# Kernel tuning notes

Hardware: AMD Instinct MI355X
Metric: run time of the kernel (lower is better)

## Reference

```python
import jax, jax.numpy as jnp
import numpy as np

B, N, DIM, HEADS, NBS = 64, 197, 768, 12, 10
WIN = (14, 14)
HEAD_DIM = DIM // HEADS
SCALE = HEAD_DIM ** -0.5


def _gen_relative_position_index():
    Wh, Ww = WIN
    num_rel = (2 * Wh - 1) * (2 * Ww - 1) + 3
    coords = np.stack(np.meshgrid(np.arange(Wh), np.arange(Ww), indexing='ij')).reshape(2, -1)
    rel = (coords[:, :, None] - coords[:, None, :]).transpose(1, 2, 0).astype(np.int32)
    rel[:, :, 0] += Wh - 1
    rel[:, :, 1] += Ww - 1
    rel[:, :, 0] *= 2 * Ww - 1
    idx = np.zeros((Wh * Ww + 1, Wh * Ww + 1), dtype=np.int32)
    idx[1:, 1:] = rel.sum(-1)
    idx[0, :] = num_rel - 3
    idx[:, 0] = num_rel - 2
    idx[0, 0] = num_rel - 1
    return jnp.asarray(idx)


def setup_inputs() -> dict:
    key = jax.random.key(0)
    ks = jax.random.split(key, 8)
    s = 0.02  # init scale for learned params
    return {
        'x': jax.random.normal(ks[0], (B, N, DIM), jnp.float32),
        'qkv_weight': jax.random.normal(ks[1], (3 * DIM, DIM), jnp.float32) * s,
        'q_bias': jax.random.normal(ks[2], (NBS, DIM), jnp.float32) * s,
        'v_bias': jax.random.normal(ks[3], (NBS, DIM), jnp.float32) * s,
        'rel_table': jax.random.normal(ks[4], (732, HEADS), jnp.float32) * s,
        'proj_weight': jax.random.normal(ks[5], (DIM, DIM), jnp.float32) * s,
        'proj_bias': jax.random.normal(ks[6], (NBS, DIM), jnp.float32) * s,
        'b_idx': jax.random.randint(ks[7], (B,), 0, NBS),
        'rel_index': _gen_relative_position_index(),
    }


def reference(x, qkv_weight, q_bias, v_bias, rel_table, proj_weight, proj_bias, b_idx, rel_index):
    Bb, Nn, C = x.shape
    # QKV projection (no fused bias), then per-sample bitfit bias (k bias is zero)
    qkv = jnp.einsum('bnc,oc->bno', x, qkv_weight)  # [B, N, 3C]
    qb = q_bias[b_idx][:, None]                     # [B, 1, C]
    vb = v_bias[b_idx][:, None]
    qkv_bias = jnp.concatenate([qb, jnp.zeros_like(qb), vb], axis=-1)
    qkv = (qkv + qkv_bias).reshape(Bb, Nn, 3, HEADS, HEAD_DIM).transpose(2, 0, 3, 1, 4)
    q, k, v = qkv[0], qkv[1], qkv[2]                # [B, H, N, d]
    attn = jnp.einsum('bhnd,bhmd->bhnm', q * SCALE, k)
    # gathered relative position bias: [H, N, N]
    rel_bias = rel_table[rel_index.reshape(-1)].reshape(Nn, Nn, HEADS).transpose(2, 0, 1)
    attn = jax.nn.softmax(attn + rel_bias[None], axis=-1)
    out = jnp.einsum('bhnm,bhmd->bhnd', attn, v)
    out = out.transpose(0, 2, 1, 3).reshape(Bb, Nn, -1)
    # output projection with per-sample bitfit bias
    out = jnp.einsum('bnc,oc->bno', out, proj_weight) + proj_bias[b_idx][:, None]
    return out
```

## Files before the change

### kernel.cpp

```cpp
#include <hip/hip_runtime.h>
#include <stdint.h>

#define B_     64
#define N_     197
#define DIM_   768
#define HEADS_ 12
#define HD_    64
#define M_     (B_*N_)
#define K3_    (3*DIM_)
#define NP_    208
#define KSTR_  72
#define VSTR_  232
#define SCALE_ 0.125f
#define GK_    768
#define NKT_   24

typedef _Float16 f16x8 __attribute__((ext_vector_type(8)));
typedef _Float16 f16x4 __attribute__((ext_vector_type(4)));
typedef _Float16 f16x2 __attribute__((ext_vector_type(2)));
typedef float    f32x4 __attribute__((ext_vector_type(4)));

__device__ __forceinline__ void gload_lds16(const void* g, void* l) {
    __builtin_amdgcn_global_load_lds(
        (const __attribute__((address_space(1))) uint32_t*)g,
        (__attribute__((address_space(3))) uint32_t*)l, 16, 0, 0);
}

__global__ __launch_bounds__(256) void cvt_f32_f16(const float* __restrict__ s,
                                                   _Float16* __restrict__ d, int n4) {
    int i = blockIdx.x * 256 + threadIdx.x;
    if (i < n4) {
        const float4 v = *(const float4*)(s + (size_t)i * 4);
        f16x4 o;
        o[0] = (_Float16)v.x; o[1] = (_Float16)v.y;
        o[2] = (_Float16)v.z; o[3] = (_Float16)v.w;
        *(f16x4*)(d + (size_t)i * 4) = o;
    }
}

__global__ __launch_bounds__(256) void biasT_pre(const int* __restrict__ rel_index,
                                                 const float* __restrict__ rel_table,
                                                 float* __restrict__ biasT) {
    int t = blockIdx.x * 256 + threadIdx.x;
    if (t < HEADS_ * NP_ * NP_) {
        int h = t / (NP_ * NP_), rem = t - h * (NP_ * NP_);
        int k = rem / NP_, q = rem - k * NP_;
        float v;
        if (k >= N_)      v = -1e30f;
        else if (q >= N_) v = 0.f;
        else              v = rel_table[rel_index[q * N_ + k] * HEADS_ + h];
        biasT[t] = v;
    }
}

template <int MODE>
__global__ __launch_bounds__(512, 2) void gemm_db(
    const _Float16* __restrict__ A, const _Float16* __restrict__ Bw,
    int M, int Nout,
    const float* __restrict__ qb, const float* __restrict__ vb,
    const float* __restrict__ pb, const int* __restrict__ b_idx,
    _Float16* __restrict__ out_h, float* __restrict__ out_f)
{
    __shared__ __align__(16) _Float16 As[3][16 * 512];
    __shared__ __align__(16) _Float16 Bs[3][8 * 512];

    const int tid  = threadIdx.x;
    const int lane = tid & 63, w = tid >> 6;
    const int wm = w >> 1, wn = w & 1;
    const int fr = lane & 15, g = lane >> 4;
    const int gl8 = ((4 * fr + g) ^ (fr >> 1)) * 8;
    const int lx = lane ^ (lane >> 3);
    const int sr = lx >> 2, sc8 = (lx & 3) * 8;

    const int gx = Nout / 128;
    const int gy = (M + 255) / 256;
    const int nwg = gx * gy;
    const int wgid = blockIdx.x + blockIdx.y * gx;
    const int q8 = nwg >> 3, r8 = nwg & 7;
    const int xcd = wgid & 7, lid = wgid >> 3;
    const int nid = (xcd < r8) ? xcd * (q8 + 1) + lid
                               : r8 * (q8 + 1) + (xcd - r8) * q8 + lid;
    const int m0 = (nid / gx) * 256, n0 = (nid % gx) * 128;

    f32x4 acc[4][4];
    #pragma unroll
    for (int i = 0; i < 4; ++i)
        #pragma unroll
        for (int j = 0; j < 4; ++j) acc[i][j] = (f32x4)0.f;

    auto stage = [&](int buf, int kt) {
        #pragma unroll
        for (int iss = 0; iss < 2; ++iss) {
            int grow = m0 + w * 32 + iss * 16 + sr;
            if (grow >= M) grow = M - 1;
            gload_lds16(A + (size_t)grow * GK_ + kt * 32 + sc8,
                        &As[buf][(2 * w + iss) * 512]);
        }
        int brow = n0 + w * 16 + sr;
        gload_lds16(Bw + (size_t)brow * GK_ + kt * 32 + sc8,
                    &Bs[buf][w * 512]);
    };

    stage(0, 0);
    stage(1, 1);

    for (int t = 0; t < NKT_; ++t) {
        if (t + 1 < NKT_) { asm volatile("s_waitcnt vmcnt(3)" ::: "memory"); }
        else              { asm volatile("s_waitcnt vmcnt(0)" ::: "memory"); }
        __builtin_amdgcn_s_barrier();
        __builtin_amdgcn_sched_barrier(0);
        if (t + 2 < NKT_) stage((t + 2) % 3, t + 2);

        const _Float16* Ac = &As[t % 3][0];
        const _Float16* Bc = &Bs[t % 3][0];
        f16x8 av[4], bv[4];
        #pragma unroll
        for (int i = 0; i < 4; ++i)
            av[i] = *(const f16x8*)&Ac[(wm * 4 + i) * 512 + gl8];
        #pragma unroll
        for (int j = 0; j < 4; ++j)
            bv[j] = *(const f16x8*)&Bc[(wn * 4 + j) * 512 + gl8];
        __builtin_amdgcn_s_setprio(1);
        #pragma unroll
        for (int i = 0; i < 4; ++i)
            #pragma unroll
            for (int j = 0; j < 4; ++j)
                acc[i][j] = __builtin_amdgcn_mfma_f32_16x16x32_f16(av[i], bv[j], acc[i][j], 0, 0, 0);
        __builtin_amdgcn_s_setprio(0);
    }

    #pragma unroll
    for (int mi = 0; mi < 4; ++mi) {
        #pragma unroll
        for (int rr = 0; rr < 4; ++rr) {
            const int row = m0 + wm * 64 + mi * 16 + g * 4 + rr;
            if (row < M) {
                const int bi = b_idx[row / N_];
                #pragma unroll
                for (int ni = 0; ni < 4; ++ni) {
                    const int col = n0 + wn * 64 + ni * 16 + fr;
                    float v = acc[mi][ni][rr];
                    if (MODE == 0) {
                        float bias = 0.f;
                        if (col < DIM_) bias = qb[bi * DIM_ + col];
                        else if (col >= 2 * DIM_) bias = vb[bi * DIM_ + (col - 2 * DIM_)];
                        out_h[(size_t)row * Nout + col] = (_Float16)(v + bias);
                    } else {
                        out_f[(size_t)row * Nout + col] = v + pb[bi * DIM_ + col];
                    }
                }
            }
        }
    }
}

__global__ __launch_bounds__(256) void attn_mfma(
    const _Float16* __restrict__ qkv, const float* __restrict__ biasT,
    _Float16* __restrict__ ctx)
{
    __shared__ __align__(16) _Float16 KP[NP_ * KSTR_];
    __shared__ __align__(16) _Float16 VT[HD_ * VSTR_];

    const int b = blockIdx.z, h = blockIdx.y, rt = blockIdx.x;
    const int r0 = rt * 64;
    const int tid = threadIdx.x, lane = tid & 63, w = tid >> 6;
    const int fr = lane & 15, g = lane >> 4;

    const size_t baseQ = (size_t)b * N_ * K3_ + h * HD_;
    const size_t baseK = baseQ + DIM_;
    const size_t baseV = baseQ + 2 * DIM_;

    for (int idx = tid; idx < NP_ * 8; idx += 256) {
        int row = idx % NP_, dc = idx / NP_;
        int gk = min(row, N_ - 1);
        f16x8 v = *(const f16x8*)(qkv + baseK + (size_t)gk * K3_ + dc * 8);
        *(f16x8*)(KP + row * KSTR_ + dc * 8) = v;
    }
    for (int idx = tid; idx < 112 * 8; idx += 256) {
        int jp = idx % 112, dc = idx / 112;
        int j0 = 2 * jp, j1 = 2 * jp + 1;
        f16x8 zz = {};
        f16x8 v0 = (j0 < N_) ? *(const f16x8*)(qkv + baseV + (size_t)j0 * K3_ + dc * 8) : zz;
        f16x8 v1 = (j1 < N_) ? *(const f16x8*)(qkv + baseV + (size_t)j1 * K3_ + dc * 8) : zz;
        #pragma unroll
        for (int e = 0; e < 8; ++e) {
            f16x2 p; p[0] = v0[e]; p[1] = v1[e];
            *(f16x2*)(VT + (dc * 8 + e) * VSTR_ + 2 * jp) = p;
        }
    }
    const int qrow = min(r0 + w * 16 + fr, N_ - 1);
    f16x8 qf[2];
    qf[0] = *(const f16x8*)(qkv + baseQ + (size_t)qrow * K3_ + g * 8);
    qf[1] = *(const f16x8*)(qkv + baseQ + (size_t)qrow * K3_ + 32 + g * 8);

    __syncthreads();

    f32x4 acc[13];
    #pragma unroll
    for (int jf = 0; jf < 13; ++jf) acc[jf] = (f32x4)0.f;
    #pragma unroll
    for (int jf = 0; jf < 13; ++jf) {
        #pragma unroll
        for (int kk = 0; kk < 2; ++kk) {
            f16x8 a = *(const f16x8*)&KP[(jf * 16 + fr) * KSTR_ + kk * 32 + g * 8];
            acc[jf] = __builtin_amdgcn_mfma_f32_16x16x32_f16(a, qf[kk], acc[jf], 0, 0, 0);
        }
    }

    const int qb_ = min(r0 + w * 16 + fr, NP_ - 1);
    const float* bp = biasT + (size_t)h * NP_ * NP_ + qb_;
    float mx = -3e38f;
    #pragma unroll
    for (int jf = 0; jf < 13; ++jf) {
        #pragma unroll
        for (int r = 0; r < 4; ++r) {
            int k = jf * 16 + g * 4 + r;
            float s = acc[jf][r] * SCALE_ + bp[(size_t)k * NP_];
            acc[jf][r] = s;
            mx = fmaxf(mx, s);
        }
    }
    mx = fmaxf(mx, __shfl_xor(mx, 16));
    mx = fmaxf(mx, __shfl_xor(mx, 32));
    float sum = 0.f;
    #pragma unroll
    for (int jf = 0; jf < 13; ++jf) {
        #pragma unroll
        for (int r = 0; r < 4; ++r) {
            float e = __expf(acc[jf][r] - mx);
            acc[jf][r] = e;
            sum += e;
        }
    }
    sum += __shfl_xor(sum, 16);
    sum += __shfl_xor(sum, 32);
    const float inv = 1.f / sum;

    __syncthreads();

    #pragma unroll
    for (int jf = 0; jf < 13; ++jf) {
        f16x4 p;
        #pragma unroll
        for (int r = 0; r < 4; ++r) p[r] = (_Float16)(acc[jf][r] * inv);
        *(f16x4*)(KP + (size_t)(w * 16 + fr) * VSTR_ + jf * 16 + g * 4) = p;
    }
    {
        f16x4 z = {};
        *(f16x4*)(KP + (size_t)(w * 16 + fr) * VSTR_ + NP_ + g * 4) = z;
    }
    __syncthreads();

    f32x4 oacc[4];
    #pragma unroll
    for (int dj = 0; dj < 4; ++dj) oacc[dj] = (f32x4)0.f;
    #pragma unroll
    for (int ks = 0; ks < 7; ++ks) {
        f16x8 a = *(const f16x8*)&KP[(size_t)(w * 16 + fr) * VSTR_ + ks * 32 + g * 8];
        #pragma unroll
        for (int dj = 0; dj < 4; ++dj) {
            f16x8 bf = *(const f16x8*)&VT[(dj * 16 + fr) * VSTR_ + ks * 32 + g * 8];
            oacc[dj] = __builtin_amdgcn_mfma_f32_16x16x32_f16(a, bf, oacc[dj], 0, 0, 0);
        }
    }
    #pragma unroll
    for (int dj = 0; dj < 4; ++dj) {
        #pragma unroll
        for (int r = 0; r < 4; ++r) {
            const int q = r0 + w * 16 + g * 4 + r;
            if (q < N_)
                ctx[((size_t)b * N_ + q) * DIM_ + h * HD_ + dj * 16 + fr] =
                    (_Float16)oacc[dj][r];
        }
    }
}

extern "C" void kernel_launch(void* const* d_in, const int* in_sizes, int n_in,
                              void* d_out, int out_size, void* d_ws, size_t ws_size,
                              hipStream_t stream) {
    const float* x     = (const float*)d_in[0];
    const float* wqkv  = (const float*)d_in[1];
    const float* qb    = (const float*)d_in[2];
    const float* vb    = (const float*)d_in[3];
    const float* rt    = (const float*)d_in[4];
    const float* wproj = (const float*)d_in[5];
    const float* pbias = (const float*)d_in[6];
    const int* b_idx   = (const int*)d_in[7];
    const int* rel_idx = (const int*)d_in[8];
    float* out = (float*)d_out;

    char* ws = (char*)d_ws;
    size_t off = 0;
    auto alloc = [&](size_t bytes) -> void* {
        void* p = ws + off; off += (bytes + 255) & ~(size_t)255; return p;
    };
    _Float16* xb    = (_Float16*)alloc((size_t)M_ * DIM_ * 2);
    _Float16* wqh   = (_Float16*)alloc((size_t)K3_ * DIM_ * 2);
    _Float16* wph   = (_Float16*)alloc((size_t)DIM_ * DIM_ * 2);
    _Float16* qkvh  = (_Float16*)alloc((size_t)M_ * K3_ * 2);
    _Float16* ctx   = (_Float16*)alloc((size_t)M_ * DIM_ * 2);
    float*    biasT = (float*)alloc((size_t)HEADS_ * NP_ * NP_ * 4);

    cvt_f32_f16<<<dim3((M_ * DIM_ / 4 + 255) / 256), 256, 0, stream>>>(x, xb, M_ * DIM_ / 4);
    cvt_f32_f16<<<dim3((K3_ * DIM_ / 4 + 255) / 256), 256, 0, stream>>>(wqkv, wqh, K3_ * DIM_ / 4);
    cvt_f32_f16<<<dim3((DIM_ * DIM_ / 4 + 255) / 256), 256, 0, stream>>>(wproj, wph, DIM_ * DIM_ / 4);
    biasT_pre<<<dim3((HEADS_ * NP_ * NP_ + 255) / 256), 256, 0, stream>>>(rel_idx, rt, biasT);

    gemm_db<0><<<dim3(K3_ / 128, (M_ + 255) / 256), 512, 0, stream>>>(
        xb, wqh, M_, K3_, qb, vb, nullptr, b_idx, qkvh, nullptr);

    attn_mfma<<<dim3(4, HEADS_, B_), 256, 0, stream>>>(qkvh, biasT, ctx);

    gemm_db<1><<<dim3(DIM_ / 128, (M_ + 255) / 256), 512, 0, stream>>>(
        ctx, wph, M_, DIM_, nullptr, nullptr, pbias, b_idx, nullptr, out);
}
```

Before: 196.6 us.

## Restructure attention kernel: 128-row tiles, direct-to-LDS swizzled K, register-shuffled P

The attention kernel now runs 512-thread blocks covering 128 query rows, which halves the redundant K/V staging per (batch, head). K is loaded with global_load_lds into a swizzled layout. The softmax probabilities no longer round-trip through LDS: they are converted and permuted into the MFMA A-operand layout with cross-lane shuffles, which removes two barriers. The cost is extra shuffle instructions and higher register pressure under launch_bounds(512,4), and more of the last row tile is wasted on padding.

```diff
diff --git a/kernel.cpp b/kernel.cpp
--- a/kernel.cpp
+++ b/kernel.cpp
@@ -9,7 +9,6 @@
 #define M_     (B_*N_)
 #define K3_    (3*DIM_)
 #define NP_    208
-#define KSTR_  72
 #define VSTR_  232
 #define SCALE_ 0.125f
 #define GK_    768
@@ -154,29 +153,34 @@
     }
 }
 
-__global__ __launch_bounds__(256) void attn_mfma(
+__global__ __launch_bounds__(512, 4) void attn_mfma(
     const _Float16* __restrict__ qkv, const float* __restrict__ biasT,
     _Float16* __restrict__ ctx)
 {
-    __shared__ __align__(16) _Float16 KP[NP_ * KSTR_];
+    __shared__ __align__(16) _Float16 Klds[26 * 512];
     __shared__ __align__(16) _Float16 VT[HD_ * VSTR_];
 
     const int b = blockIdx.z, h = blockIdx.y, rt = blockIdx.x;
-    const int r0 = rt * 64;
+    const int r0 = rt * 128;
     const int tid = threadIdx.x, lane = tid & 63, w = tid >> 6;
     const int fr = lane & 15, g = lane >> 4;
+    const int gl8 = ((4 * fr + g) ^ (fr >> 1)) * 8;
 
     const size_t baseQ = (size_t)b * N_ * K3_ + h * HD_;
     const size_t baseK = baseQ + DIM_;
     const size_t baseV = baseQ + 2 * DIM_;
 
-    for (int idx = tid; idx < NP_ * 8; idx += 256) {
-        int row = idx % NP_, dc = idx / NP_;
-        int gk = min(row, N_ - 1);
-        f16x8 v = *(const f16x8*)(qkv + baseK + (size_t)gk * K3_ + dc * 8);
-        *(f16x8*)(KP + row * KSTR_ + dc * 8) = v;
-    }
-    for (int idx = tid; idx < 112 * 8; idx += 256) {
+    {
+        const int l = lane ^ (lane >> 3);
+        const int cr = l >> 2, cc = (l & 3) * 8;
+        for (int c = w; c < 26; c += 8) {
+            const int jf = c >> 1, kk = c & 1;
+            int grow = jf * 16 + cr; if (grow > N_ - 1) grow = N_ - 1;
+            gload_lds16(qkv + baseK + (size_t)grow * K3_ + kk * 32 + cc,
+                        &Klds[c * 512]);
+        }
+    }
+    for (int idx = tid; idx < 112 * 8; idx += 512) {
         int jp = idx % 112, dc = idx / 112;
         int j0 = 2 * jp, j1 = 2 * jp + 1;
         f16x8 zz = {};
@@ -188,22 +192,22 @@
             *(f16x2*)(VT + (dc * 8 + e) * VSTR_ + 2 * jp) = p;
         }
     }
-    const int qrow = min(r0 + w * 16 + fr, N_ - 1);
+    int qrow = r0 + w * 16 + fr; if (qrow > N_ - 1) qrow = N_ - 1;
     f16x8 qf[2];
     qf[0] = *(const f16x8*)(qkv + baseQ + (size_t)qrow * K3_ + g * 8);
     qf[1] = *(const f16x8*)(qkv + baseQ + (size_t)qrow * K3_ + 32 + g * 8);
 
     __syncthreads();
 
-    f32x4 acc[13];
-    #pragma unroll
-    for (int jf = 0; jf < 13; ++jf) acc[jf] = (f32x4)0.f;
+    f32x4 p[13];
+    #pragma unroll
+    for (int jf = 0; jf < 13; ++jf) p[jf] = (f32x4)0.f;
     #pragma unroll
     for (int jf = 0; jf < 13; ++jf) {
         #pragma unroll
         for (int kk = 0; kk < 2; ++kk) {
-            f16x8 a = *(const f16x8*)&KP[(jf * 16 + fr) * KSTR_ + kk * 32 + g * 8];
-            acc[jf] = __builtin_amdgcn_mfma_f32_16x16x32_f16(a, qf[kk], acc[jf], 0, 0, 0);
+            f16x8 a = *(const f16x8*)&Klds[(jf * 2 + kk) * 512 + gl8];
+            p[jf] = __builtin_amdgcn_mfma_f32_16x16x32_f16(a, qf[kk], p[jf], 0, 0, 0);
         }
     }
 
@@ -215,8 +219,8 @@
         #pragma unroll
         for (int r = 0; r < 4; ++r) {
             int k = jf * 16 + g * 4 + r;
-            float s = acc[jf][r] * SCALE_ + bp[(size_t)k * NP_];
-            acc[jf][r] = s;
+            float s = p[jf][r] * SCALE_ + bp[(size_t)k * NP_];
+            p[jf][r] = s;
             mx = fmaxf(mx, s);
         }
     }
@@ -227,8 +231,8 @@
     for (int jf = 0; jf < 13; ++jf) {
         #pragma unroll
         for (int r = 0; r < 4; ++r) {
-            float e = __expf(acc[jf][r] - mx);
-            acc[jf][r] = e;
+            float e = __expf(p[jf][r] - mx);
+            p[jf][r] = e;
             sum += e;
         }
     }
@@ -236,33 +240,48 @@
     sum += __shfl_xor(sum, 32);
     const float inv = 1.f / sum;
 
-    __syncthreads();
-
-    #pragma unroll
-    for (int jf = 0; jf < 13; ++jf) {
-        f16x4 p;
-        #pragma unroll
-        for (int r = 0; r < 4; ++r) p[r] = (_Float16)(acc[jf][r] * inv);
-        *(f16x4*)(KP + (size_t)(w * 16 + fr) * VSTR_ + jf * 16 + g * 4) = p;
-    }
-    {
-        f16x4 z = {};
-        *(f16x4*)(KP + (size_t)(w * 16 + fr) * VSTR_ + NP_ + g * 4) = z;
-    }
-    __syncthreads();
-
+    const int src0 = ((2 * g) & 3) * 16 + fr;
+    const int src1 = ((2 * g + 1) & 3) * 16 + fr;
+    const bool hi = (g >= 2);
     f32x4 oacc[4];
     #pragma unroll
     for (int dj = 0; dj < 4; ++dj) oacc[dj] = (f32x4)0.f;
+
     #pragma unroll
     for (int ks = 0; ks < 7; ++ks) {
-        f16x8 a = *(const f16x8*)&KP[(size_t)(w * 16 + fr) * VSTR_ + ks * 32 + g * 8];
+        f16x2 t;
+        t[0] = (_Float16)(p[2 * ks][0] * inv); t[1] = (_Float16)(p[2 * ks][1] * inv);
+        uint32_t a01 = __builtin_bit_cast(uint32_t, t);
+        t[0] = (_Float16)(p[2 * ks][2] * inv); t[1] = (_Float16)(p[2 * ks][3] * inv);
+        uint32_t a23 = __builtin_bit_cast(uint32_t, t);
+        uint32_t b01 = 0, b23 = 0;
+        if (ks < 6) {
+            t[0] = (_Float16)(p[2 * ks + 1][0] * inv); t[1] = (_Float16)(p[2 * ks + 1][1] * inv);
+            b01 = __builtin_bit_cast(uint32_t, t);
+            t[0] = (_Float16)(p[2 * ks + 1][2] * inv); t[1] = (_Float16)(p[2 * ks + 1][3] * inv);
+            b23 = __builtin_bit_cast(uint32_t, t);
+        }
+        uint32_t xa, xb;
+        uint32_t wd[4];
+        xa = (uint32_t)__shfl((int)a01, src0); xb = (uint32_t)__shfl((int)b01, src0);
+        wd[0] = hi ? xb : xa;
+        xa = (uint32_t)__shfl((int)a23, src0); xb = (uint32_t)__shfl((int)b23, src0);
+        wd[1] = hi ? xb : xa;
+        xa = (uint32_t)__shfl((int)a01, src1); xb = (uint32_t)__shfl((int)b01, src1);
+        wd[2] = hi ? xb : xa;
+        xa = (uint32_t)__shfl((int)a23, src1); xb = (uint32_t)__shfl((int)b23, src1);
+        wd[3] = hi ? xb : xa;
+        typedef uint32_t u32x4 __attribute__((ext_vector_type(4)));
+        u32x4 wv; wv[0] = wd[0]; wv[1] = wd[1]; wv[2] = wd[2]; wv[3] = wd[3];
+        f16x8 af = __builtin_bit_cast(f16x8, wv);
+
         #pragma unroll
         for (int dj = 0; dj < 4; ++dj) {
             f16x8 bf = *(const f16x8*)&VT[(dj * 16 + fr) * VSTR_ + ks * 32 + g * 8];
-            oacc[dj] = __builtin_amdgcn_mfma_f32_16x16x32_f16(a, bf, oacc[dj], 0, 0, 0);
-        }
-    }
+            oacc[dj] = __builtin_amdgcn_mfma_f32_16x16x32_f16(af, bf, oacc[dj], 0, 0, 0);
+        }
+    }
+
     #pragma unroll
     for (int dj = 0; dj < 4; ++dj) {
         #pragma unroll
@@ -309,7 +328,7 @@
     gemm_db<0><<<dim3(K3_ / 128, (M_ + 255) / 256), 512, 0, stream>>>(
         xb, wqh, M_, K3_, qb, vb, nullptr, b_idx, qkvh, nullptr);
 
-    attn_mfma<<<dim3(4, HEADS_, B_), 256, 0, stream>>>(qkvh, biasT, ctx);
+    attn_mfma<<<dim3(2, HEADS_, B_), 512, 0, stream>>>(qkvh, biasT, ctx);
 
     gemm_db<1><<<dim3(DIM_ / 128, (M_ + 255) / 256), 512, 0, stream>>>(
         ctx, wph, M_, DIM_, nullptr, nullptr, pbias, b_idx, nullptr, out);
```

New measurement: 169.7 us. 13.7% less time.
